# Kernel optimization log

Measured on AMD Instinct MI355X. Metric: run time of the kernel, lower is better.

Reference implementation:

```python
import jax, jax.numpy as jnp
import numpy as np

N = 50000
E = 800000
C_IN, C_HID, C_OUT = 512, 128, 2
HEADS2 = 3
NEG_SLOPE = 0.2


def gat_conv(x, src, dst, W, att_src, att_dst, bias, heads, ch, concat):
    """PyG GATConv (eval mode) on pre-augmented (self-loop included) edge lists.
    x: [N, F_in], W: [F_in, heads*ch], att_*: [heads, ch], bias: [heads*ch] or [ch].
    """
    n = x.shape[0]
    h = (x @ W).reshape(n, heads, ch)                 # [N, H, C]
    a_src = (h * att_src).sum(-1)                     # [N, H]
    a_dst = (h * att_dst).sum(-1)                     # [N, H]
    e = jax.nn.leaky_relu(a_src[src] + a_dst[dst], NEG_SLOPE)  # [E', H]
    # segment softmax over edges sharing a destination node
    m = jax.ops.segment_max(e, dst, num_segments=n)
    m = jnp.where(jnp.isfinite(m), m, 0.0)
    ex = jnp.exp(e - m[dst])
    denom = jax.ops.segment_sum(ex, dst, num_segments=n)
    alpha = ex / (denom[dst] + 1e-16)                 # [E', H]
    out = jax.ops.segment_sum(h[src] * alpha[:, :, None], dst, num_segments=n)  # [N, H, C]
    out = out.reshape(n, heads * ch) if concat else out.mean(axis=1)
    return out + bias


def setup_inputs() -> dict:
    key = jax.random.key(0)
    ks = jax.random.split(key, 12)
    x = jax.random.normal(ks[0], (N, C_IN), dtype=jnp.float32)
    edge_index = jax.random.randint(ks[1], (2, E), 0, N, dtype=jnp.int64)
    s1 = 1.0 / np.sqrt(C_IN)
    s2 = 1.0 / np.sqrt(C_HID)
    return {
        "x": x,
        "edge_index": edge_index,
        "W1": jax.random.normal(ks[2], (C_IN, C_HID), dtype=jnp.float32) * s1,
        "att_src1": jax.random.normal(ks[3], (1, C_HID), dtype=jnp.float32) * s2,
        "att_dst1": jax.random.normal(ks[4], (1, C_HID), dtype=jnp.float32) * s2,
        "bias1": jnp.zeros((C_HID,), dtype=jnp.float32),
        "W2": jax.random.normal(ks[5], (C_HID, HEADS2 * C_OUT), dtype=jnp.float32) * s2,
        "att_src2": jax.random.normal(ks[6], (HEADS2, C_OUT), dtype=jnp.float32) * 0.5,
        "att_dst2": jax.random.normal(ks[7], (HEADS2, C_OUT), dtype=jnp.float32) * 0.5,
        "bias2": jnp.zeros((C_OUT,), dtype=jnp.float32),
    }


def reference(x, edge_index, W1, att_src1, att_dst1, bias1, W2, att_src2, att_dst2, bias2):
    n = x.shape[0]
    loop = jnp.arange(n, dtype=edge_index.dtype)
    src = jnp.concatenate([edge_index[0], loop])      # PyG add_self_loops=True
    dst = jnp.concatenate([edge_index[1], loop])
    h = gat_conv(x, src, dst, W1, att_src1, att_dst1, bias1, 1, C_HID, True)
    h = jax.nn.relu(h)                                # Dropout is identity in eval
    out = gat_conv(h, src, dst, W2, att_src2, att_dst2, bias2, HEADS2, C_OUT, False)
    return out
```

## Files before the change

kernel.cpp:

```cpp
#include <hip/hip_runtime.h>

#define N_NODES 50000
#define N_EDGES 800000
#define E_TOT   850000
#define C_IN    512
#define C_HID   128
#define NEG     0.2f

typedef _Float16 f16x8 __attribute__((ext_vector_type(8)));
typedef __attribute__((ext_vector_type(4))) float f32x4;

__device__ __forceinline__ float leaky(float x) { return x > 0.f ? x : NEG * x; }

union U32H2 { unsigned u; _Float16 h[2]; float f; };
union BFrag { uint4 u; f16x8 h; };

__device__ __forceinline__ unsigned short f2h(float f) {
  U32H2 c; c.h[0] = (_Float16)f; return (unsigned short)(c.u & 0xffff);
}

__device__ __forceinline__ unsigned pk2h(float a, float b) {
  union { __fp16 v __attribute__((ext_vector_type(2))); unsigned u; } c;
  c.v = __builtin_amdgcn_cvt_pkrtz(a, b);
  return c.u;
}

__device__ __forceinline__ float row_reduce_add(float v) {
  union { float f; int i; } a, b;
  a.f = v;
  b.i = __builtin_amdgcn_update_dpp(0, a.i, 0xB1, 0xF, 0xF, true);  a.f += b.f;
  b.i = __builtin_amdgcn_update_dpp(0, a.i, 0x4E, 0xF, 0xF, true);  a.f += b.f;
  b.i = __builtin_amdgcn_update_dpp(0, a.i, 0x124, 0xF, 0xF, true); a.f += b.f;
  b.i = __builtin_amdgcn_update_dpp(0, a.i, 0x128, 0xF, 0xF, true); a.f += b.f;
  return a.f;
}

__global__ __launch_bounds__(256) void setup_kernel(
    const float* __restrict__ W1, const float* __restrict__ as1,
    const float* __restrict__ ad1, const int* __restrict__ ei,
    unsigned short* __restrict__ Wswz, float* __restrict__ v1s, float* __restrict__ v1d,
    int* __restrict__ deg, int* __restrict__ rnk) {
  const int b = blockIdx.x;
  if (b < 32) {
    int t = b * 256 + threadIdx.x;
    int c = t >> 6, kc = t & 63;
    if (c >= C_HID) return;
    int kblk = kc >> 2, q = kc & 3;
    int ct = c >> 4, l15 = c & 15;
    int lane = q * 16 + l15;
    unsigned short hb[8], lb[8];
#pragma unroll
    for (int i = 0; i < 8; i++) {
      float w = W1[(size_t)(kc * 8 + i) * C_HID + c];
      _Float16 hi = (_Float16)w;
      _Float16 lo = (_Float16)(w - (float)hi);
      U32H2 ch; ch.h[0] = hi;
      U32H2 cl; cl.h[0] = lo;
      hb[i] = (unsigned short)(ch.u & 0xffff);
      lb[i] = (unsigned short)(cl.u & 0xffff);
    }
    size_t chunk0 = ((size_t)(kblk * 8 + ct) * 2) * 512;
    *(uint4*)&Wswz[chunk0 + (size_t)lane * 8]       = *(uint4*)hb;
    *(uint4*)&Wswz[chunk0 + 512 + (size_t)lane * 8] = *(uint4*)lb;
  } else if (b < 160) {
    const int wv = threadIdx.x >> 6, lane = threadIdx.x & 63;
    const int k = (b - 32) * 4 + wv;
    if (k >= C_IN) return;
    float2 w = *(const float2*)(W1 + (size_t)k * C_HID + 2 * lane);
    float2 a = *(const float2*)(as1 + 2 * lane);
    float2 d = *(const float2*)(ad1 + 2 * lane);
    float s = w.x * a.x + w.y * a.y;
    float t = w.x * d.x + w.y * d.y;
#pragma unroll
    for (int m = 32; m >= 1; m >>= 1) {
      s += __shfl_xor(s, m, 64);
      t += __shfl_xor(t, m, 64);
    }
    if (lane == 0) { v1s[k] = s; v1d[k] = t; }
  } else {
    int e = (b - 160) * 256 + threadIdx.x;
    if (e < N_EDGES) rnk[e] = atomicAdd(&deg[ei[N_EDGES + e]], 1);
  }
}

__global__ __launch_bounds__(256, 3) void lin1_kernel(const float* __restrict__ x,
    const unsigned short* __restrict__ Wswz,
    const float* __restrict__ v1s, const float* __restrict__ v1d,
    unsigned short* __restrict__ h1u, float* __restrict__ a_src, float* __restrict__ a_dst,
    const int* __restrict__ deg, int* __restrict__ rowptr) {
  __shared__ __attribute__((aligned(16))) unsigned short As[2][4][64][40];
  __shared__ int wsum[4];

  if (blockIdx.x == 0) {
    const int tid = threadIdx.x, lane = tid & 63, wv = tid >> 6;
    int carry = 0;
    for (int base = 0; base < N_NODES; base += 8192) {
      int i0 = base + tid * 32;
      int v[32];
      if (i0 + 32 <= N_NODES) {
#pragma unroll
        for (int k = 0; k < 8; k++) {
          int4 t4 = *(const int4*)(deg + i0 + 4 * k);
          v[4 * k]     = t4.x + 1; v[4 * k + 1] = t4.y + 1;
          v[4 * k + 2] = t4.z + 1; v[4 * k + 3] = t4.w + 1;
        }
      } else {
#pragma unroll
        for (int k = 0; k < 32; k++) v[k] = (i0 + k < N_NODES) ? deg[i0 + k] + 1 : 0;
      }
      int tsum = 0;
#pragma unroll
      for (int k = 0; k < 32; k++) tsum += v[k];
      int sc = tsum;
#pragma unroll
      for (int off = 1; off < 64; off <<= 1) {
        int t = __shfl_up(sc, off, 64);
        if (lane >= off) sc += t;
      }
      if (lane == 63) wsum[wv] = sc;
      __syncthreads();
      if (tid < 4) {
        int s = wsum[tid];
#pragma unroll
        for (int off = 1; off < 4; off <<= 1) {
          int t = __shfl_up(s, off, 64);
          if (tid >= off) s += t;
        }
        wsum[tid] = s;
      }
      __syncthreads();
      int run = carry + (wv ? wsum[wv - 1] : 0) + sc - tsum;
      if (i0 + 32 <= N_NODES) {
#pragma unroll
        for (int k = 0; k < 8; k++) {
          int4 w4;
          w4.x = run; run += v[4 * k];
          w4.y = run; run += v[4 * k + 1];
          w4.z = run; run += v[4 * k + 2];
          w4.w = run; run += v[4 * k + 3];
          *(int4*)(rowptr + i0 + 4 * k) = w4;
        }
      } else {
#pragma unroll
        for (int k = 0; k < 32; k++) {
          if (i0 + k < N_NODES) rowptr[i0 + k] = run;
          run += v[k];
        }
      }
      carry += wsum[3];
      __syncthreads();
    }
    if (tid == 0) rowptr[N_NODES] = carry;
    return;
  }

  const int tid  = threadIdx.x;
  const int lane = tid & 63, wv = tid >> 6;
  const int m0   = (blockIdx.x - 1) * 64;

  const int arow = tid >> 2, kseg = (tid & 3) * 8;
  int grow = m0 + arow;
  if (grow >= N_NODES) grow = N_NODES - 1;
  const float* xrow = x + (size_t)grow * C_IN + kseg;

  f32x4 acc[4][2];
#pragma unroll
  for (int rt = 0; rt < 4; rt++) { acc[rt][0] = (f32x4)0.f; acc[rt][1] = (f32x4)0.f; }
  float ps = 0.f, pd = 0.f;

  const int q = lane >> 4, l15 = lane & 15;

  float4 xp[4][2];
#pragma unroll
  for (int s = 0; s < 4; s++) {
    xp[s][0] = *(const float4*)(xrow + s * 32);
    xp[s][1] = *(const float4*)(xrow + s * 32 + 4);
  }

#pragma unroll
  for (int kb = 0; kb < 4; kb++) {
    const int k0 = kb * 128;
    const int buf = kb & 1;
#pragma unroll
    for (int s = 0; s < 4; s++) {
      float4 vsa = *(const float4*)(v1s + k0 + s * 32 + kseg);
      float4 vsb = *(const float4*)(v1s + k0 + s * 32 + kseg + 4);
      float4 vda = *(const float4*)(v1d + k0 + s * 32 + kseg);
      float4 vdb = *(const float4*)(v1d + k0 + s * 32 + kseg + 4);
      ps += xp[s][0].x * vsa.x + xp[s][0].y * vsa.y + xp[s][0].z * vsa.z + xp[s][0].w * vsa.w
          + xp[s][1].x * vsb.x + xp[s][1].y * vsb.y + xp[s][1].z * vsb.z + xp[s][1].w * vsb.w;
      pd += xp[s][0].x * vda.x + xp[s][0].y * vda.y + xp[s][0].z * vda.z + xp[s][0].w * vda.w
          + xp[s][1].x * vdb.x + xp[s][1].y * vdb.y + xp[s][1].z * vdb.z + xp[s][1].w * vdb.w;
      *(uint4*)&As[buf][s][arow][kseg] =
          make_uint4(pk2h(xp[s][0].x, xp[s][0].y), pk2h(xp[s][0].z, xp[s][0].w),
                     pk2h(xp[s][1].x, xp[s][1].y), pk2h(xp[s][1].z, xp[s][1].w));
    }
    __syncthreads();
    if (kb < 3) {
#pragma unroll
      for (int s = 0; s < 4; s++) {
        xp[s][0] = *(const float4*)(xrow + k0 + 128 + s * 32);
        xp[s][1] = *(const float4*)(xrow + k0 + 128 + s * 32 + 4);
      }
    }

#pragma unroll
    for (int sp = 0; sp < 2; sp++) {
      BFrag bf[2][4];
#pragma unroll
      for (int s = 0; s < 2; s++) {
        const int sub = sp * 2 + s;
        const unsigned short* bp =
            Wswz + ((size_t)((kb * 4 + sub) * 8 + wv * 2) * 2) * 512 + (size_t)lane * 8;
        bf[s][0].u = *(const uint4*)(bp);
        bf[s][1].u = *(const uint4*)(bp + 512);
        bf[s][2].u = *(const uint4*)(bp + 1024);
        bf[s][3].u = *(const uint4*)(bp + 1536);
      }
#pragma unroll
      for (int rt = 0; rt < 4; rt++) {
#pragma unroll
        for (int s = 0; s < 2; s++) {
          const int sub = sp * 2 + s;
          f16x8 af = *(const f16x8*)&As[buf][sub][rt * 16 + l15][q * 8];
          acc[rt][0] = __builtin_amdgcn_mfma_f32_16x16x32_f16(af, bf[s][0].h, acc[rt][0], 0, 0, 0);
          acc[rt][0] = __builtin_amdgcn_mfma_f32_16x16x32_f16(af, bf[s][1].h, acc[rt][0], 0, 0, 0);
          acc[rt][1] = __builtin_amdgcn_mfma_f32_16x16x32_f16(af, bf[s][2].h, acc[rt][1], 0, 0, 0);
          acc[rt][1] = __builtin_amdgcn_mfma_f32_16x16x32_f16(af, bf[s][3].h, acc[rt][1], 0, 0, 0);
        }
      }
    }
  }

  ps += __shfl_xor(ps, 1, 64); ps += __shfl_xor(ps, 2, 64);
  pd += __shfl_xor(pd, 1, 64); pd += __shfl_xor(pd, 2, 64);
  if ((tid & 3) == 0) {
    int row = m0 + arow;
    if (row < N_NODES) { a_src[row] = ps; a_dst[row] = pd; }
  }

#pragma unroll
  for (int rt = 0; rt < 4; rt++) {
    int rbase = m0 + rt * 16 + q * 4;
#pragma unroll
    for (int ct = 0; ct < 2; ct++) {
      int col = wv * 32 + ct * 16 + l15;
#pragma unroll
      for (int ri = 0; ri < 4; ri++) {
        int row = rbase + ri;
        if (row < N_NODES)
          h1u[(size_t)row * C_HID + col] = f2h(acc[rt][ct][ri]);
      }
    }
  }
}

__global__ void bucket_kernel(const int* __restrict__ ei, const int* __restrict__ rnk,
                              const int* __restrict__ rowptr,
                              const float* __restrict__ a_src, const float* __restrict__ a_dst,
                              int2* __restrict__ esw) {
  int e = blockIdx.x * blockDim.x + threadIdx.x;
  if (e >= E_TOT) return;
  int src, slot;
  if (e < N_EDGES) {
    src = ei[e];
    int dst = ei[N_EDGES + e];
    slot = rowptr[dst] + rnk[e];
    U32H2 c; c.f = __expf(leaky(a_src[src] + a_dst[dst]));
    esw[slot] = make_int2(src, (int)c.u);
  } else {
    int n = e - N_EDGES;
    slot = rowptr[n + 1] - 1;
    U32H2 c; c.f = __expf(leaky(a_src[n] + a_dst[n]));
    esw[slot] = make_int2(n, (int)c.u);
  }
}

__global__ __launch_bounds__(256) void agg1_kernel(const unsigned short* __restrict__ h1u,
    const int2* __restrict__ esw, const int* __restrict__ rowptr,
    const float* __restrict__ bias1, const float* __restrict__ W2,
    const float* __restrict__ as2w, const float* __restrict__ ad2w,
    float* __restrict__ hs2) {
  const int wv = threadIdx.x >> 6, lane = threadIdx.x & 63;
  const int r = lane & 15;
  const int n = blockIdx.x * 16 + wv * 4 + (lane >> 4);
  const int start = rowptr[n], end = rowptr[n + 1];

  const unsigned short* hbase = h1u + r * 8;

  float acc[8] = {0, 0, 0, 0, 0, 0, 0, 0};
  float wsum = 0.f;

  int base = start;
  int cnt = min(end - base, 8);
  int2 rec[8];
#pragma unroll
  for (int j = 0; j < 8; j++) rec[j] = esw[j < cnt ? base + j : base];

  while (true) {
    const int nbase = base + 8;
    const bool more = nbase < end;
    int ncnt = 0;
    int2 nrec[8];
    if (more) {
      ncnt = min(end - nbase, 8);
#pragma unroll
      for (int j = 0; j < 8; j++) nrec[j] = esw[j < ncnt ? nbase + j : nbase];
    }
    uint4 g[8];
#pragma unroll
    for (int j = 0; j < 8; j++)
      g[j] = *(const uint4*)(hbase + (size_t)rec[j].x * C_HID);
#pragma unroll
    for (int j = 0; j < 8; j++) {
      U32H2 cw; cw.u = (unsigned)rec[j].y;
      const float W = (j < cnt) ? cw.f : 0.f;
      wsum += W;
      U32H2 c0, c1, c2, c3;
      c0.u = g[j].x; c1.u = g[j].y; c2.u = g[j].z; c3.u = g[j].w;
      acc[0] = fmaf(W, (float)c0.h[0], acc[0]); acc[1] = fmaf(W, (float)c0.h[1], acc[1]);
      acc[2] = fmaf(W, (float)c1.h[0], acc[2]); acc[3] = fmaf(W, (float)c1.h[1], acc[3]);
      acc[4] = fmaf(W, (float)c2.h[0], acc[4]); acc[5] = fmaf(W, (float)c2.h[1], acc[5]);
      acc[6] = fmaf(W, (float)c3.h[0], acc[6]); acc[7] = fmaf(W, (float)c3.h[1], acc[7]);
    }
    if (!more) break;
    base = nbase; cnt = ncnt;
#pragma unroll
    for (int j = 0; j < 8; j++) rec[j] = nrec[j];
  }

  const float inv = 1.f / wsum;

  float4 ba = *(const float4*)(bias1 + r * 8);
  float4 bb = *(const float4*)(bias1 + r * 8 + 4);
  float u[8] = {fmaxf(acc[0] * inv + ba.x, 0.f), fmaxf(acc[1] * inv + ba.y, 0.f),
                fmaxf(acc[2] * inv + ba.z, 0.f), fmaxf(acc[3] * inv + ba.w, 0.f),
                fmaxf(acc[4] * inv + bb.x, 0.f), fmaxf(acc[5] * inv + bb.y, 0.f),
                fmaxf(acc[6] * inv + bb.z, 0.f), fmaxf(acc[7] * inv + bb.w, 0.f)};
  float p[6] = {0, 0, 0, 0, 0, 0};
#pragma unroll
  for (int j = 0; j < 8; j++) {
    const float* w2r = W2 + (size_t)(r * 8 + j) * 6;
#pragma unroll
    for (int o = 0; o < 6; o++) p[o] = fmaf(u[j], w2r[o], p[o]);
  }
#pragma unroll
  for (int o = 0; o < 6; o++) p[o] = row_reduce_add(p[o]);

  if (r == 0) {
    float as0 = p[0] * as2w[0] + p[1] * as2w[1];
    float as1 = p[2] * as2w[2] + p[3] * as2w[3];
    float as2_ = p[4] * as2w[4] + p[5] * as2w[5];
    float ad0 = p[0] * ad2w[0] + p[1] * ad2w[1];
    float ad1 = p[2] * ad2w[2] + p[3] * ad2w[3];
    float ad2_ = p[4] * ad2w[4] + p[5] * ad2w[5];
    float* dst = hs2 + (size_t)n * 12;
    *(float4*)(dst)     = make_float4(p[0], p[1], p[2], p[3]);
    *(float4*)(dst + 4) = make_float4(p[4], p[5], as0, as1);
    *(float4*)(dst + 8) = make_float4(as2_, ad0, ad1, ad2_);
  }
}

__global__ __launch_bounds__(256) void agg2_kernel(const float* __restrict__ hs2,
    const int* __restrict__ rowptr, const int2* __restrict__ esw,
    const float* __restrict__ bias2, float* __restrict__ out) {
  const int wv = threadIdx.x >> 6, lane = threadIdx.x & 63;
  const int q = lane >> 4, r = lane & 15;
  const int n = blockIdx.x * 16 + wv * 4 + q;
  if (n >= N_NODES) return;
  const int start = rowptr[n], end = rowptr[n + 1];
  float4 own = *(const float4*)(hs2 + (size_t)n * 12 + 8);
  const float ad0 = own.y, ad1 = own.z, ad2 = own.w;

  float d0 = 0.f, d1 = 0.f, d2 = 0.f;
  float a0 = 0.f, a1 = 0.f, a2 = 0.f, a3 = 0.f, a4 = 0.f, a5 = 0.f;
  for (int j = start + r; j < end; j += 32) {
    const int jb = j + 16;
    const bool h1 = jb < end;
    int s0 = esw[j].x;
    int s1 = esw[h1 ? jb : j].x;
    const float* r0 = hs2 + (size_t)s0 * 12;
    const float* r1 = hs2 + (size_t)s1 * 12;
    float4 A0 = *(const float4*)(r0);
    float4 B0 = *(const float4*)(r0 + 4);
    float  C0 = r0[8];
    float4 A1 = *(const float4*)(r1);
    float4 B1 = *(const float4*)(r1 + 4);
    float  C1 = r1[8];
    {
      float e0 = __expf(leaky(B0.z + ad0));
      float e1 = __expf(leaky(B0.w + ad1));
      float e2 = __expf(leaky(C0 + ad2));
      d0 += e0; d1 += e1; d2 += e2;
      a0 += e0 * A0.x; a1 += e0 * A0.y;
      a2 += e1 * A0.z; a3 += e1 * A0.w;
      a4 += e2 * B0.x; a5 += e2 * B0.y;
    }
    if (h1) {
      float e0 = __expf(leaky(B1.z + ad0));
      float e1 = __expf(leaky(B1.w + ad1));
      float e2 = __expf(leaky(C1 + ad2));
      d0 += e0; d1 += e1; d2 += e2;
      a0 += e0 * A1.x; a1 += e0 * A1.y;
      a2 += e1 * A1.z; a3 += e1 * A1.w;
      a4 += e2 * B1.x; a5 += e2 * B1.y;
    }
  }
  d0 = row_reduce_add(d0); d1 = row_reduce_add(d1); d2 = row_reduce_add(d2);
  a0 = row_reduce_add(a0); a1 = row_reduce_add(a1); a2 = row_reduce_add(a2);
  a3 = row_reduce_add(a3); a4 = row_reduce_add(a4); a5 = row_reduce_add(a5);
  if (r == 0) {
    float o0 = (a0 / d0 + a2 / d1 + a4 / d2) * (1.f / 3.f) + bias2[0];
    float o1 = (a1 / d0 + a3 / d1 + a5 / d2) * (1.f / 3.f) + bias2[1];
    *(float2*)(out + (size_t)n * 2) = make_float2(o0, o1);
  }
}

extern "C" void kernel_launch(void* const* d_in, const int* in_sizes, int n_in,
                              void* d_out, int out_size, void* d_ws, size_t ws_size,
                              hipStream_t stream) {
  const float* x        = (const float*)d_in[0];
  const int*   ei       = (const int*)d_in[1];
  const float* W1       = (const float*)d_in[2];
  const float* att_src1 = (const float*)d_in[3];
  const float* att_dst1 = (const float*)d_in[4];
  const float* bias1    = (const float*)d_in[5];
  const float* W2       = (const float*)d_in[6];
  const float* att_src2 = (const float*)d_in[7];
  const float* att_dst2 = (const float*)d_in[8];
  const float* bias2    = (const float*)d_in[9];
  float* out = (float*)d_out;

  char* w = (char*)d_ws;
  auto alloc = [&](size_t bytes) {
    char* p = w;
    w += (bytes + 255) & ~(size_t)255;
    return p;
  };
  unsigned short* h1u    = (unsigned short*)alloc((size_t)N_NODES * C_HID * 2);
  unsigned short* Wswz   = (unsigned short*)alloc((size_t)C_IN * C_HID * 2 * 2);
  float*          v1s    = (float*)alloc((size_t)C_IN * 4);
  float*          v1d    = (float*)alloc((size_t)C_IN * 4);
  float*          a_src1 = (float*)alloc((size_t)N_NODES * 4);
  float*          a_dst1 = (float*)alloc((size_t)N_NODES * 4);
  int*            deg    = (int*)alloc((size_t)N_NODES * 4);
  int*            rowptr = (int*)alloc((size_t)(N_NODES + 4) * 4);
  int*            rnk    = (int*)alloc((size_t)N_EDGES * 4);
  int2*           esw    = (int2*)alloc((size_t)E_TOT * 8);
  float*          hs2    = (float*)alloc((size_t)N_NODES * 12 * 4);

  (void)hipMemsetAsync(deg, 0, (size_t)N_NODES * 4, stream);

  setup_kernel<<<160 + (N_EDGES + 255) / 256, 256, 0, stream>>>(
      W1, att_src1, att_dst1, ei, Wswz, v1s, v1d, deg, rnk);
  lin1_kernel<<<(N_NODES + 63) / 64 + 1, 256, 0, stream>>>(x, Wswz, v1s, v1d,
                                                           h1u, a_src1, a_dst1,
                                                           deg, rowptr);
  bucket_kernel<<<(E_TOT + 255) / 256, 256, 0, stream>>>(ei, rnk, rowptr,
                                                         a_src1, a_dst1, esw);
  agg1_kernel<<<N_NODES / 16, 256, 0, stream>>>(h1u, esw, rowptr, bias1, W2,
                                                att_src2, att_dst2, hs2);
  agg2_kernel<<<(N_NODES + 15) / 16, 256, 0, stream>>>(hs2, rowptr, esw, bias2, out);
}
```

Before: 290.5 us.

## Overlap degree counting with GEMM blocks and single-buffer LDS tile

Moves the per-edge degree/rank atomic counting out of the setup kernel and into extra blocks of the lin1 GEMM launch. Block 0, which builds the row pointer scan, now spins on a completion counter until all degree blocks finish, so the edge atomics run alongside the GEMM instead of before it. The LDS A tile becomes single-buffered with an extra barrier per k-step, and launch bounds rise to 4 waves per SIMD to raise occupancy. The risks are block 0 spinning while the degree blocks wait to be scheduled, the added barrier stalls, and more register pressure under the tighter launch bound.

```diff
diff --git a/kernel.cpp b/kernel.cpp
--- a/kernel.cpp
+++ b/kernel.cpp
@@ -6,6 +6,9 @@
 #define C_IN    512
 #define C_HID   128
 #define NEG     0.2f
+
+#define GEMM_BLKS 782
+#define DR_BLKS   256
 
 typedef _Float16 f16x8 __attribute__((ext_vector_type(8)));
 typedef __attribute__((ext_vector_type(4))) float f32x4;
@@ -37,9 +40,8 @@
 
 __global__ __launch_bounds__(256) void setup_kernel(
     const float* __restrict__ W1, const float* __restrict__ as1,
-    const float* __restrict__ ad1, const int* __restrict__ ei,
-    unsigned short* __restrict__ Wswz, float* __restrict__ v1s, float* __restrict__ v1d,
-    int* __restrict__ deg, int* __restrict__ rnk) {
+    const float* __restrict__ ad1,
+    unsigned short* __restrict__ Wswz, float* __restrict__ v1s, float* __restrict__ v1d) {
   const int b = blockIdx.x;
   if (b < 32) {
     int t = b * 256 + threadIdx.x;
@@ -62,7 +64,7 @@
     size_t chunk0 = ((size_t)(kblk * 8 + ct) * 2) * 512;
     *(uint4*)&Wswz[chunk0 + (size_t)lane * 8]       = *(uint4*)hb;
     *(uint4*)&Wswz[chunk0 + 512 + (size_t)lane * 8] = *(uint4*)lb;
-  } else if (b < 160) {
+  } else {
     const int wv = threadIdx.x >> 6, lane = threadIdx.x & 63;
     const int k = (b - 32) * 4 + wv;
     if (k >= C_IN) return;
@@ -77,36 +79,47 @@
       t += __shfl_xor(t, m, 64);
     }
     if (lane == 0) { v1s[k] = s; v1d[k] = t; }
-  } else {
-    int e = (b - 160) * 256 + threadIdx.x;
-    if (e < N_EDGES) rnk[e] = atomicAdd(&deg[ei[N_EDGES + e]], 1);
-  }
-}
-
-__global__ __launch_bounds__(256, 3) void lin1_kernel(const float* __restrict__ x,
+  }
+}
+
+__global__ __launch_bounds__(256, 4) void lin1_kernel(const float* __restrict__ x,
     const unsigned short* __restrict__ Wswz,
     const float* __restrict__ v1s, const float* __restrict__ v1d,
     unsigned short* __restrict__ h1u, float* __restrict__ a_src, float* __restrict__ a_dst,
-    const int* __restrict__ deg, int* __restrict__ rowptr) {
-  __shared__ __attribute__((aligned(16))) unsigned short As[2][4][64][40];
+    int* __restrict__ deg, int* __restrict__ rowptr,
+    const int* __restrict__ ei, int* __restrict__ rnk, int* __restrict__ dctr) {
+  __shared__ __attribute__((aligned(16))) unsigned short As[4][64][40];
   __shared__ int wsum[4];
 
-  if (blockIdx.x == 0) {
+  const int b = blockIdx.x;
+
+  if (b > GEMM_BLKS) {
+    const int tid = threadIdx.x;
+    const int bb = b - 1 - GEMM_BLKS;
+    for (int e = bb * 256 + tid; e < N_EDGES; e += DR_BLKS * 256)
+      rnk[e] = atomicAdd(&deg[ei[N_EDGES + e]], 1);
+    __syncthreads();
+    if (tid == 0) { __threadfence(); atomicAdd(dctr, 1); }
+    return;
+  }
+
+  if (b == 0) {
     const int tid = threadIdx.x, lane = tid & 63, wv = tid >> 6;
+    if (tid == 0) {
+      while (__hip_atomic_load(dctr, __ATOMIC_ACQUIRE, __HIP_MEMORY_SCOPE_AGENT) < DR_BLKS)
+        __builtin_amdgcn_s_sleep(32);
+    }
+    __syncthreads();
     int carry = 0;
     for (int base = 0; base < N_NODES; base += 8192) {
       int i0 = base + tid * 32;
       int v[32];
-      if (i0 + 32 <= N_NODES) {
-#pragma unroll
-        for (int k = 0; k < 8; k++) {
-          int4 t4 = *(const int4*)(deg + i0 + 4 * k);
-          v[4 * k]     = t4.x + 1; v[4 * k + 1] = t4.y + 1;
-          v[4 * k + 2] = t4.z + 1; v[4 * k + 3] = t4.w + 1;
-        }
-      } else {
-#pragma unroll
-        for (int k = 0; k < 32; k++) v[k] = (i0 + k < N_NODES) ? deg[i0 + k] + 1 : 0;
+#pragma unroll
+      for (int k = 0; k < 32; k++) {
+        int idx = i0 + k;
+        v[k] = (idx < N_NODES)
+            ? __hip_atomic_load(&deg[idx], __ATOMIC_RELAXED, __HIP_MEMORY_SCOPE_AGENT) + 1
+            : 0;
       }
       int tsum = 0;
 #pragma unroll
@@ -156,7 +169,7 @@
 
   const int tid  = threadIdx.x;
   const int lane = tid & 63, wv = tid >> 6;
-  const int m0   = (blockIdx.x - 1) * 64;
+  const int m0   = (b - 1) * 64;
 
   const int arow = tid >> 2, kseg = (tid & 3) * 8;
   int grow = m0 + arow;
@@ -180,7 +193,7 @@
 #pragma unroll
   for (int kb = 0; kb < 4; kb++) {
     const int k0 = kb * 128;
-    const int buf = kb & 1;
+    if (kb > 0) __syncthreads();
 #pragma unroll
     for (int s = 0; s < 4; s++) {
       float4 vsa = *(const float4*)(v1s + k0 + s * 32 + kseg);
@@ -191,7 +204,7 @@
           + xp[s][1].x * vsb.x + xp[s][1].y * vsb.y + xp[s][1].z * vsb.z + xp[s][1].w * vsb.w;
       pd += xp[s][0].x * vda.x + xp[s][0].y * vda.y + xp[s][0].z * vda.z + xp[s][0].w * vda.w
           + xp[s][1].x * vdb.x + xp[s][1].y * vdb.y + xp[s][1].z * vdb.z + xp[s][1].w * vdb.w;
-      *(uint4*)&As[buf][s][arow][kseg] =
+      *(uint4*)&As[s][arow][kseg] =
           make_uint4(pk2h(xp[s][0].x, xp[s][0].y), pk2h(xp[s][0].z, xp[s][0].w),
                      pk2h(xp[s][1].x, xp[s][1].y), pk2h(xp[s][1].z, xp[s][1].w));
     }
@@ -205,29 +218,21 @@
     }
 
 #pragma unroll
-    for (int sp = 0; sp < 2; sp++) {
-      BFrag bf[2][4];
-#pragma unroll
-      for (int s = 0; s < 2; s++) {
-        const int sub = sp * 2 + s;
-        const unsigned short* bp =
-            Wswz + ((size_t)((kb * 4 + sub) * 8 + wv * 2) * 2) * 512 + (size_t)lane * 8;
-        bf[s][0].u = *(const uint4*)(bp);
-        bf[s][1].u = *(const uint4*)(bp + 512);
-        bf[s][2].u = *(const uint4*)(bp + 1024);
-        bf[s][3].u = *(const uint4*)(bp + 1536);
-      }
+    for (int sub = 0; sub < 4; sub++) {
+      const unsigned short* bp =
+          Wswz + ((size_t)((kb * 4 + sub) * 8 + wv * 2) * 2) * 512 + (size_t)lane * 8;
+      BFrag b00, b01, b10, b11;
+      b00.u = *(const uint4*)(bp);
+      b01.u = *(const uint4*)(bp + 512);
+      b10.u = *(const uint4*)(bp + 1024);
+      b11.u = *(const uint4*)(bp + 1536);
 #pragma unroll
       for (int rt = 0; rt < 4; rt++) {
-#pragma unroll
-        for (int s = 0; s < 2; s++) {
-          const int sub = sp * 2 + s;
-          f16x8 af = *(const f16x8*)&As[buf][sub][rt * 16 + l15][q * 8];
-          acc[rt][0] = __builtin_amdgcn_mfma_f32_16x16x32_f16(af, bf[s][0].h, acc[rt][0], 0, 0, 0);
-          acc[rt][0] = __builtin_amdgcn_mfma_f32_16x16x32_f16(af, bf[s][1].h, acc[rt][0], 0, 0, 0);
-          acc[rt][1] = __builtin_amdgcn_mfma_f32_16x16x32_f16(af, bf[s][2].h, acc[rt][1], 0, 0, 0);
-          acc[rt][1] = __builtin_amdgcn_mfma_f32_16x16x32_f16(af, bf[s][3].h, acc[rt][1], 0, 0, 0);
-        }
+        f16x8 af = *(const f16x8*)&As[sub][rt * 16 + l15][q * 8];
+        acc[rt][0] = __builtin_amdgcn_mfma_f32_16x16x32_f16(af, b00.h, acc[rt][0], 0, 0, 0);
+        acc[rt][0] = __builtin_amdgcn_mfma_f32_16x16x32_f16(af, b01.h, acc[rt][0], 0, 0, 0);
+        acc[rt][1] = __builtin_amdgcn_mfma_f32_16x16x32_f16(af, b10.h, acc[rt][1], 0, 0, 0);
+        acc[rt][1] = __builtin_amdgcn_mfma_f32_16x16x32_f16(af, b11.h, acc[rt][1], 0, 0, 0);
       }
     }
   }
@@ -444,18 +449,17 @@
   float*          a_src1 = (float*)alloc((size_t)N_NODES * 4);
   float*          a_dst1 = (float*)alloc((size_t)N_NODES * 4);
   int*            deg    = (int*)alloc((size_t)N_NODES * 4);
+  int*            dctr   = (int*)alloc(256);
   int*            rowptr = (int*)alloc((size_t)(N_NODES + 4) * 4);
   int*            rnk    = (int*)alloc((size_t)N_EDGES * 4);
   int2*           esw    = (int2*)alloc((size_t)E_TOT * 8);
   float*          hs2    = (float*)alloc((size_t)N_NODES * 12 * 4);
 
-  (void)hipMemsetAsync(deg, 0, (size_t)N_NODES * 4, stream);
-
-  setup_kernel<<<160 + (N_EDGES + 255) / 256, 256, 0, stream>>>(
-      W1, att_src1, att_dst1, ei, Wswz, v1s, v1d, deg, rnk);
-  lin1_kernel<<<(N_NODES + 63) / 64 + 1, 256, 0, stream>>>(x, Wswz, v1s, v1d,
-                                                           h1u, a_src1, a_dst1,
-                                                           deg, rowptr);
+  (void)hipMemsetAsync(deg, 0, ((size_t)N_NODES * 4 + 255 & ~(size_t)255) + 256, stream);
+
+  setup_kernel<<<160, 256, 0, stream>>>(W1, att_src1, att_dst1, Wswz, v1s, v1d);
+  lin1_kernel<<<1 + GEMM_BLKS + DR_BLKS, 256, 0, stream>>>(
+      x, Wswz, v1s, v1d, h1u, a_src1, a_dst1, deg, rowptr, ei, rnk, dctr);
   bucket_kernel<<<(E_TOT + 255) / 256, 256, 0, stream>>>(ei, rnk, rowptr,
                                                          a_src1, a_dst1, esw);
   agg1_kernel<<<N_NODES / 16, 256, 0, stream>>>(h1u, esw, rowptr, bias1, W2,
```

Result: slower. 324.2 us (+11.6%).
